# Kernel optimization log

Hardware: AMD Instinct MI355X
Metric: run time of the kernel (lower is better)

Reference implementation:

```python
import jax, jax.numpy as jnp
import numpy as np

EMB = 1536   # emb_dim
RANK = 32
N3 = 204     # modules with in_dim=3840 (6 per layer x 34 layers)
N10 = 34     # modules with in_dim=10240 (1 per layer x 34 layers)


def setup_inputs() -> dict:
    key = jax.random.key(0)
    ks = jax.random.split(key, 9)
    s = lambda k, shp: jax.random.normal(k, shp, dtype=jnp.float32)
    return {
        "x": s(ks[0], (EMB,)),
        "Wp3": s(ks[1], (N3, RANK * RANK, EMB)) * 0.02,   # stacked proj.weight for d=3840 group
        "bp3": s(ks[2], (N3, RANK * RANK)) * 0.02,        # stacked proj.bias
        "Wp10": s(ks[3], (N10, RANK * RANK, EMB)) * 0.02,
        "bp10": s(ks[4], (N10, RANK * RANK)) * 0.02,
        "A3": s(ks[5], (N3, RANK, 3840)),                 # stacked lora_a (rank, in_dim)
        "A10": s(ks[6], (N10, RANK, 10240)),
        "B3": s(ks[7], (N3, 3840, RANK)),                 # stacked lora_b (out_dim, rank); out_dim=3840 group
        "B10": s(ks[8], (N10, 10240, RANK)),
    }


def reference(x, Wp3, bp3, Wp10, bp10, A3, A10, B3, B10):
    # Batched version of the per-module torch loop:
    #   P = proj(x).view(rank, rank);  lora_a_out = P @ lora_a;  lora_b_out = lora_b
    # proj is a GEMV per module -> batched as one einsum per in_dim group.
    P3 = (jnp.einsum('nke,e->nk', Wp3, x) + bp3).reshape(N3, RANK, RANK)    # [N3,32,32]
    P10 = (jnp.einsum('nke,e->nk', Wp10, x) + bp10).reshape(N10, RANK, RANK)  # [N10,32,32]
    la3 = jnp.einsum('nij,njd->nid', P3, A3)      # [N3,32,3840]
    la10 = jnp.einsum('nij,njd->nid', P10, A10)   # [N10,32,10240]
    # lora_b weights are returned unchanged (pass-through), as in the torch module.
    return (la3, la10, B3, B10)
```

## Files before the change

kernel.cpp:

```cpp
#include <hip/hip_runtime.h>

#define EMB   1536
#define RANK  32
#define RANK2 1024
#define N3    204
#define N10   34
#define D3    3840
#define D10   10240

__global__ void gemv_kernel(const float* __restrict__ W,
                            const float* __restrict__ b,
                            const float* __restrict__ x,
                            float* __restrict__ P,
                            int total_rows) {
    const int wavesPerBlock = blockDim.x >> 6;
    const int row  = blockIdx.x * wavesPerBlock + (threadIdx.x >> 6);
    const int lane = threadIdx.x & 63;
    if (row >= total_rows) return;

    const float* w = W + (size_t)row * EMB;
    float acc = 0.f;
#pragma unroll
    for (int it = 0; it < EMB / 256; ++it) {
        const int e = (it * 64 + lane) * 4;
        const float4 wv = *reinterpret_cast<const float4*>(w + e);
        const float4 xv = *reinterpret_cast<const float4*>(x + e);
        acc = fmaf(wv.x, xv.x, acc);
        acc = fmaf(wv.y, xv.y, acc);
        acc = fmaf(wv.z, xv.z, acc);
        acc = fmaf(wv.w, xv.w, acc);
    }
#pragma unroll
    for (int off = 32; off > 0; off >>= 1)
        acc += __shfl_down(acc, off);
    if (lane == 0) P[row] = acc + b[row];
}

__global__ void pa_kernel(const float* __restrict__ P,
                          const float* __restrict__ A,
                          float* __restrict__ out,
                          int D, int blocksPerModule) {
    const int module = blockIdx.x / blocksPerModule;
    const int dblk   = blockIdx.x % blocksPerModule;
    const int d      = dblk * blockDim.x + threadIdx.x;

    __shared__ float Ps[RANK2];
    for (int i = threadIdx.x; i < RANK2; i += blockDim.x)
        Ps[i] = P[(size_t)module * RANK2 + i];
    __syncthreads();

    if (d >= D) return;

    const float* a = A + (size_t)module * RANK * D + d;
    float av[RANK];
#pragma unroll
    for (int j = 0; j < RANK; ++j)
        av[j] = a[(size_t)j * D];

    float* o = out + (size_t)module * RANK * D + d;
#pragma unroll
    for (int i = 0; i < RANK; ++i) {
        float acc = 0.f;
#pragma unroll
        for (int j = 0; j < RANK; ++j)
            acc = fmaf(Ps[i * RANK + j], av[j], acc);
        o[(size_t)i * D] = acc;
    }
}

extern "C" void kernel_launch(void* const* d_in, const int* in_sizes, int n_in,
                              void* d_out, int out_size, void* d_ws, size_t ws_size,
                              hipStream_t stream) {
    const float* x    = (const float*)d_in[0];
    const float* Wp3  = (const float*)d_in[1];
    const float* bp3  = (const float*)d_in[2];
    const float* Wp10 = (const float*)d_in[3];
    const float* bp10 = (const float*)d_in[4];
    const float* A3   = (const float*)d_in[5];
    const float* A10  = (const float*)d_in[6];
    const float* B3   = (const float*)d_in[7];
    const float* B10  = (const float*)d_in[8];

    float* out = (float*)d_out;

    float* P3  = (float*)d_ws;
    float* P10 = P3 + (size_t)N3 * RANK2;

    const size_t SZ_LA3  = (size_t)N3  * RANK * D3;
    const size_t SZ_LA10 = (size_t)N10 * RANK * D10;

    float* la3  = out;
    float* la10 = out + SZ_LA3;
    float* oB3  = la10 + SZ_LA10;
    float* oB10 = oB3 + SZ_LA3;

    {
        const int rows3 = N3 * RANK2;
        const int rows10 = N10 * RANK2;
        gemv_kernel<<<rows3 / 4, 256, 0, stream>>>(Wp3, bp3, x, P3, rows3);
        gemv_kernel<<<rows10 / 4, 256, 0, stream>>>(Wp10, bp10, x, P10, rows10);
    }

    {
        const int bpm3  = D3 / 256;
        const int bpm10 = D10 / 256;
        pa_kernel<<<N3 * bpm3, 256, 0, stream>>>(P3, A3, la3, D3, bpm3);
        pa_kernel<<<N10 * bpm10, 256, 0, stream>>>(P10, A10, la10, D10, bpm10);
    }

    hipMemcpyAsync(oB3,  B3,  SZ_LA3  * sizeof(float), hipMemcpyDeviceToDevice, stream);
    hipMemcpyAsync(oB10, B10, SZ_LA10 * sizeof(float), hipMemcpyDeviceToDevice, stream);
}
```

Before: 382.1 us.

## Merge GEMV launches and fuse P@A with B pass-through copies into one kernel

The two per-group GEMV launches become one kernel that selects its group by wave index. The two P@A kernels and the two device-to-device memcpys become a single launch whose blocks are split into P@A work and float4 copy work. This removes launch overhead and the serialization between the P@A and copy stages, so the copy bandwidth can overlap with the P@A traffic. The cost is a more complex block dispatch and no longer relying on the driver's memcpy path.

```diff
diff --git a/kernel.cpp b/kernel.cpp
--- a/kernel.cpp
+++ b/kernel.cpp
@@ -8,15 +8,40 @@
 #define D3    3840
 #define D10   10240
 
-__global__ void gemv_kernel(const float* __restrict__ W,
-                            const float* __restrict__ b,
-                            const float* __restrict__ x,
-                            float* __restrict__ P,
-                            int total_rows) {
-    const int wavesPerBlock = blockDim.x >> 6;
-    const int row  = blockIdx.x * wavesPerBlock + (threadIdx.x >> 6);
+#define ROWS3  (N3 * RANK2)
+#define ROWS10 (N10 * RANK2)
+
+#define BPM3   (D3 / 256)
+#define BPM10  (D10 / 256)
+#define PA3_BLOCKS  (N3 * BPM3)
+#define PA10_BLOCKS (N10 * BPM10)
+
+#define SZ_LA3  ((size_t)N3  * RANK * D3)
+#define SZ_LA10 ((size_t)N10 * RANK * D10)
+
+#define CP_F4_PER_BLOCK 4096
+#define CP3_BLOCKS  ((int)(SZ_LA3  / 4 / CP_F4_PER_BLOCK))
+#define CP10_BLOCKS ((int)(SZ_LA10 / 4 / CP_F4_PER_BLOCK))
+
+__global__ void gemv_all(const float* __restrict__ W3,
+                         const float* __restrict__ b3,
+                         const float* __restrict__ W10,
+                         const float* __restrict__ b10,
+                         const float* __restrict__ x,
+                         float* __restrict__ P3,
+                         float* __restrict__ P10) {
+    const int wave = blockIdx.x * (blockDim.x >> 6) + (threadIdx.x >> 6);
     const int lane = threadIdx.x & 63;
-    if (row >= total_rows) return;
+
+    const float* W;
+    const float* b;
+    float* P;
+    int row;
+    if (wave < ROWS3) {
+        W = W3; b = b3; P = P3; row = wave;
+    } else {
+        W = W10; b = b10; P = P10; row = wave - ROWS3;
+    }
 
     const float* w = W + (size_t)row * EMB;
     float acc = 0.f;
@@ -36,21 +61,16 @@
     if (lane == 0) P[row] = acc + b[row];
 }
 
-__global__ void pa_kernel(const float* __restrict__ P,
-                          const float* __restrict__ A,
-                          float* __restrict__ out,
-                          int D, int blocksPerModule) {
-    const int module = blockIdx.x / blocksPerModule;
-    const int dblk   = blockIdx.x % blocksPerModule;
-    const int d      = dblk * blockDim.x + threadIdx.x;
-
+__device__ __forceinline__ void pa_block(const float* __restrict__ P,
+                                         const float* __restrict__ A,
+                                         float* __restrict__ out,
+                                         int module, int dblk, int D) {
     __shared__ float Ps[RANK2];
     for (int i = threadIdx.x; i < RANK2; i += blockDim.x)
         Ps[i] = P[(size_t)module * RANK2 + i];
     __syncthreads();
 
-    if (d >= D) return;
-
+    const int d = dblk * blockDim.x + threadIdx.x;
     const float* a = A + (size_t)module * RANK * D + d;
     float av[RANK];
 #pragma unroll
@@ -66,6 +86,44 @@
             acc = fmaf(Ps[i * RANK + j], av[j], acc);
         o[(size_t)i * D] = acc;
     }
+}
+
+__device__ __forceinline__ void copy_block(const float4* __restrict__ src,
+                                           float4* __restrict__ dst,
+                                           int chunk) {
+    const size_t base = (size_t)chunk * CP_F4_PER_BLOCK + threadIdx.x;
+#pragma unroll
+    for (int it = 0; it < CP_F4_PER_BLOCK / 256; ++it)
+        dst[base + it * 256] = src[base + it * 256];
+}
+
+__global__ void fused_b(const float* __restrict__ P3,
+                        const float* __restrict__ A3,
+                        float* __restrict__ la3,
+                        const float* __restrict__ P10,
+                        const float* __restrict__ A10,
+                        float* __restrict__ la10,
+                        const float4* __restrict__ B3,
+                        float4* __restrict__ oB3,
+                        const float4* __restrict__ B10,
+                        float4* __restrict__ oB10) {
+    int bid = blockIdx.x;
+    if (bid < PA3_BLOCKS) {
+        pa_block(P3, A3, la3, bid / BPM3, bid % BPM3, D3);
+        return;
+    }
+    bid -= PA3_BLOCKS;
+    if (bid < PA10_BLOCKS) {
+        pa_block(P10, A10, la10, bid / BPM10, bid % BPM10, D10);
+        return;
+    }
+    bid -= PA10_BLOCKS;
+    if (bid < CP3_BLOCKS) {
+        copy_block(B3, oB3, bid);
+        return;
+    }
+    bid -= CP3_BLOCKS;
+    copy_block(B10, oB10, bid);
 }
 
 extern "C" void kernel_launch(void* const* d_in, const int* in_sizes, int n_in,
@@ -86,28 +144,17 @@
     float* P3  = (float*)d_ws;
     float* P10 = P3 + (size_t)N3 * RANK2;
 
-    const size_t SZ_LA3  = (size_t)N3  * RANK * D3;
-    const size_t SZ_LA10 = (size_t)N10 * RANK * D10;
-
     float* la3  = out;
     float* la10 = out + SZ_LA3;
     float* oB3  = la10 + SZ_LA10;
     float* oB10 = oB3 + SZ_LA3;
 
-    {
-        const int rows3 = N3 * RANK2;
-        const int rows10 = N10 * RANK2;
-        gemv_kernel<<<rows3 / 4, 256, 0, stream>>>(Wp3, bp3, x, P3, rows3);
-        gemv_kernel<<<rows10 / 4, 256, 0, stream>>>(Wp10, bp10, x, P10, rows10);
-    }
+    gemv_all<<<(ROWS3 + ROWS10) / 4, 256, 0, stream>>>(
+        Wp3, bp3, Wp10, bp10, x, P3, P10);
 
-    {
-        const int bpm3  = D3 / 256;
-        const int bpm10 = D10 / 256;
-        pa_kernel<<<N3 * bpm3, 256, 0, stream>>>(P3, A3, la3, D3, bpm3);
-        pa_kernel<<<N10 * bpm10, 256, 0, stream>>>(P10, A10, la10, D10, bpm10);
-    }
-
-    hipMemcpyAsync(oB3,  B3,  SZ_LA3  * sizeof(float), hipMemcpyDeviceToDevice, stream);
-    hipMemcpyAsync(oB10, B10, SZ_LA10 * sizeof(float), hipMemcpyDeviceToDevice, stream);
+    const int total_blocks = PA3_BLOCKS + PA10_BLOCKS + CP3_BLOCKS + CP10_BLOCKS;
+    fused_b<<<total_blocks, 256, 0, stream>>>(
+        P3, A3, la3, P10, A10, la10,
+        (const float4*)B3, (float4*)oB3,
+        (const float4*)B10, (float4*)oB10);
 }
```

Result: faster. 367.6 us (-3.8%).
